# Kernel optimization log

Measured on AMD Instinct MI355X. Metric: run time of the kernel, lower is better.

## Reference

```python
import jax, jax.numpy as jnp
import numpy as np

B, S, D, H = 4, 2048, 1024, 16
DK = D // H

def setup_inputs() -> dict:
    key = jax.random.key(0)
    ks = jax.random.split(key, 8)
    Q = jax.random.normal(ks[0], (B, S, D), dtype=jnp.float32)
    K = jax.random.normal(ks[1], (B, S, D), dtype=jnp.float32)
    V = jax.random.normal(ks[2], (B, S, D), dtype=jnp.float32)
    # causal mask: 0 means masked (as in masked_fill(mask == 0, -inf))
    mask = jnp.broadcast_to(jnp.tril(jnp.ones((S, S), dtype=jnp.int32))[None, None], (B, 1, S, S))
    scale = 1.0 / np.sqrt(D)
    W_Q = jax.random.normal(ks[3], (D, D), dtype=jnp.float32) * scale
    W_K = jax.random.normal(ks[4], (D, D), dtype=jnp.float32) * scale
    W_V = jax.random.normal(ks[5], (D, D), dtype=jnp.float32) * scale
    W_O = jax.random.normal(ks[6], (D, D), dtype=jnp.float32) * scale
    return {"Q": Q, "K": K, "V": V, "mask": mask,
            "W_Q": W_Q, "W_K": W_K, "W_V": W_V, "W_O": W_O}

def _split_heads(x):
    # [B, S, D] -> [B, H, S, DK]
    b, s, _ = x.shape
    return x.reshape(b, s, H, DK).transpose(0, 2, 1, 3)

def reference(Q, K, V, mask, W_Q, W_K, W_V, W_O):
    # nn.Linear(d,d,bias=False): y = x @ W.T ; here W_* stored as [D, D]
    q = _split_heads(Q @ W_Q.T)
    k = _split_heads(K @ W_K.T)
    v = _split_heads(V @ W_V.T)
    scores = jnp.einsum('bhqd,bhkd->bhqk', q, k) / jnp.sqrt(jnp.float32(DK))
    scores = jnp.where(mask == 0, -jnp.inf, scores)
    weights = jax.nn.softmax(scores, axis=-1)
    weights = jnp.nan_to_num(weights, nan=0.0)  # fully-masked rows -> 0
    # dropout is identity at eval / p=0
    attn = jnp.einsum('bhqk,bhkd->bhqd', weights, v)
    attn = attn.transpose(0, 2, 1, 3).reshape(Q.shape[0], Q.shape[1], D)
    return attn @ W_O.T
```

## Files before the change

kernel.cpp:

```cpp
#include <hip/hip_runtime.h>
#include <stdint.h>

#define B_  4
#define S_  2048
#define D_  1024
#define H_  16
#define DK_ 64

typedef __attribute__((ext_vector_type(8)))  short   short8;
typedef __attribute__((ext_vector_type(8)))  unsigned short ushort8;
typedef __attribute__((ext_vector_type(4)))  float   f32x4;
typedef __attribute__((ext_vector_type(16))) float   f32x16;

#define GPTR(p) ((const __attribute__((address_space(1))) void*)(p))
#define SPTR(p) ((__attribute__((address_space(3))) void*)(p))

__device__ inline unsigned short f2bf(float f) {
  uint32_t u = __float_as_uint(f);
  uint32_t r = (u + 0x7fffu + ((u >> 16) & 1u)) >> 16;
  return (unsigned short)r;
}
__device__ inline float bf2f(unsigned short h) {
  return __uint_as_float(((uint32_t)h) << 16);
}
__device__ inline uint32_t pkbf(float a, float b) {
  uint32_t r;
  asm("v_cvt_pk_bf16_f32 %0, %1, %2" : "=v"(r) : "v"(a), "v"(b));
  return r;
}
__device__ inline short8 mk8(uint32_t a, uint32_t b, uint32_t c, uint32_t d) {
  union { uint32_t u[4]; short8 s; } x;
  x.u[0] = a; x.u[1] = b; x.u[2] = c; x.u[3] = d;
  return x.s;
}

__global__ __launch_bounds__(256) void conv_one(const float* __restrict__ src,
                                                unsigned short* __restrict__ dst,
                                                size_t n) {
  size_t i = ((size_t)blockIdx.x * blockDim.x + threadIdx.x) * 4;
  if (i < n) {
    float4 v = *reinterpret_cast<const float4*>(src + i);
    ushort4 o;
    o.x = f2bf(v.x); o.y = f2bf(v.y); o.z = f2bf(v.z); o.w = f2bf(v.w);
    *reinterpret_cast<ushort4*>(dst + i) = o;
  }
}

__global__ __launch_bounds__(256) void conv_x3(const float* __restrict__ q,
                                               const float* __restrict__ k,
                                               const float* __restrict__ v,
                                               unsigned short* __restrict__ dst) {
  const size_t NX = (size_t)B_ * S_ * D_;
  const float* src = (blockIdx.z == 0) ? q : (blockIdx.z == 1) ? k : v;
  unsigned short* d = dst + (size_t)blockIdx.z * NX;
  size_t i = ((size_t)blockIdx.x * blockDim.x + threadIdx.x) * 4;
  float4 vv = *reinterpret_cast<const float4*>(src + i);
  ushort4 o;
  o.x = f2bf(vv.x); o.y = f2bf(vv.y); o.z = f2bf(vv.z); o.w = f2bf(vv.w);
  *reinterpret_cast<ushort4*>(d + i) = o;
}

__global__ __launch_bounds__(256) void conv_w4(const float* __restrict__ w0,
                                               const float* __restrict__ w1,
                                               const float* __restrict__ w2,
                                               const float* __restrict__ w3,
                                               unsigned short* __restrict__ dst) {
  const size_t NW = (size_t)D_ * D_;
  const float* src = (blockIdx.z == 0) ? w0 : (blockIdx.z == 1) ? w1
                   : (blockIdx.z == 2) ? w2 : w3;
  unsigned short* d = dst + (size_t)blockIdx.z * NW;
  size_t i = ((size_t)blockIdx.x * blockDim.x + threadIdx.x) * 4;
  if (i < NW) {
    float4 v = *reinterpret_cast<const float4*>(src + i);
    ushort4 o;
    o.x = f2bf(v.x); o.y = f2bf(v.y); o.z = f2bf(v.z); o.w = f2bf(v.w);
    *reinterpret_cast<ushort4*>(d + i) = o;
  }
}

#define BM 128
#define BN 128
#define BK 32

__global__ __launch_bounds__(256) void gemm_qkv(const unsigned short* __restrict__ X0,
                                                const unsigned short* __restrict__ X1,
                                                const unsigned short* __restrict__ X2,
                                                const unsigned short* __restrict__ W,
                                                unsigned short* __restrict__ P,
                                                int zbase) {
  const size_t NW = (size_t)D_ * D_;
  const size_t NX = (size_t)B_ * S_ * D_;
  const int z = zbase + blockIdx.z;

  const unsigned short* A;
  const unsigned short* Bm;
  unsigned short* C;
  int N, m0, n0;
  if (z == 2) {
    A = W + 2 * NW; Bm = X2; C = P + 2 * NX;
    N = B_ * S_;
    m0 = (blockIdx.x & 7) * BM;
    n0 = (blockIdx.x >> 3) * BN;
  } else {
    A = z ? X1 : X0; Bm = W + (size_t)z * NW; C = P + (size_t)z * NX;
    N = D_;
    m0 = (blockIdx.x >> 3) * BM;
    n0 = (blockIdx.x & 7) * BN;
  }
  const int K = D_;

  __shared__ unsigned short sA[BM * BK];
  __shared__ unsigned short sB[BN * BK];

  const int tid  = threadIdx.x;
  const int lane = tid & 63;
  const int wid  = tid >> 6;
  const int wr   = wid >> 1, wc = wid & 1;
  const int g = lane >> 4, c = lane & 15;

  f32x4 acc[4][4];
#pragma unroll
  for (int m = 0; m < 4; ++m)
#pragma unroll
    for (int n = 0; n < 4; ++n) acc[m][n] = (f32x4){0.f, 0.f, 0.f, 0.f};

  const int nkt = K / BK;
  for (int kt = 0; kt < nkt; ++kt) {
    const int k0 = kt * BK;
#pragma unroll
    for (int i = 0; i < 2; ++i) {
      const int ob  = i * 4096 + wid * 1024 + lane * 16;
      const int row = ob >> 6;
      const int cb  = ob & 63;
      const unsigned short* ga = A  + (size_t)(m0 + row) * K + k0 + (cb >> 1);
      const unsigned short* gb = Bm + (size_t)(n0 + row) * K + k0 + (cb >> 1);
      __builtin_amdgcn_global_load_lds(GPTR(ga), SPTR(&sA[(i * 4096 + wid * 1024) >> 1]), 16, 0, 0);
      __builtin_amdgcn_global_load_lds(GPTR(gb), SPTR(&sB[(i * 4096 + wid * 1024) >> 1]), 16, 0, 0);
    }
    __syncthreads();

    short8 af[4], bf[4];
#pragma unroll
    for (int m = 0; m < 4; ++m)
      af[m] = *reinterpret_cast<const short8*>(&sA[(wr * 64 + m * 16 + c) * BK + 8 * g]);
#pragma unroll
    for (int n = 0; n < 4; ++n)
      bf[n] = *reinterpret_cast<const short8*>(&sB[(wc * 64 + n * 16 + c) * BK + 8 * g]);
#pragma unroll
    for (int m = 0; m < 4; ++m)
#pragma unroll
      for (int n = 0; n < 4; ++n)
        acc[m][n] = __builtin_amdgcn_mfma_f32_16x16x32_bf16(af[m], bf[n], acc[m][n], 0, 0, 0);
    __syncthreads();
  }

#pragma unroll
  for (int m = 0; m < 4; ++m)
#pragma unroll
    for (int n = 0; n < 4; ++n)
#pragma unroll
      for (int r = 0; r < 4; ++r) {
        const int row = m0 + wr * 64 + m * 16 + 4 * g + r;
        const int col = n0 + wc * 64 + n * 16 + c;
        C[(size_t)row * N + col] = f2bf(acc[m][n][r]);
      }
}

__global__ __launch_bounds__(256) void gemm_out(const unsigned short* __restrict__ A,
                                                const unsigned short* __restrict__ Bm,
                                                float* __restrict__ C,
                                                int M, int N, int K) {
  __shared__ unsigned short sA[BM * BK];
  __shared__ unsigned short sB[BN * BK];

  const int tid  = threadIdx.x;
  const int lane = tid & 63;
  const int wid  = tid >> 6;
  const int wr   = wid >> 1, wc = wid & 1;
  const int g = lane >> 4, c = lane & 15;

  const int m0 = blockIdx.y * BM;
  const int n0 = blockIdx.x * BN;

  f32x4 acc[4][4];
#pragma unroll
  for (int m = 0; m < 4; ++m)
#pragma unroll
    for (int n = 0; n < 4; ++n) acc[m][n] = (f32x4){0.f, 0.f, 0.f, 0.f};

  const int nkt = K / BK;
  for (int kt = 0; kt < nkt; ++kt) {
    const int k0 = kt * BK;
#pragma unroll
    for (int i = 0; i < 2; ++i) {
      const int ob  = i * 4096 + wid * 1024 + lane * 16;
      const int row = ob >> 6;
      const int cb  = ob & 63;
      const unsigned short* ga = A  + (size_t)(m0 + row) * K + k0 + (cb >> 1);
      const unsigned short* gb = Bm + (size_t)(n0 + row) * K + k0 + (cb >> 1);
      __builtin_amdgcn_global_load_lds(GPTR(ga), SPTR(&sA[(i * 4096 + wid * 1024) >> 1]), 16, 0, 0);
      __builtin_amdgcn_global_load_lds(GPTR(gb), SPTR(&sB[(i * 4096 + wid * 1024) >> 1]), 16, 0, 0);
    }
    __syncthreads();

    short8 af[4], bf[4];
#pragma unroll
    for (int m = 0; m < 4; ++m)
      af[m] = *reinterpret_cast<const short8*>(&sA[(wr * 64 + m * 16 + c) * BK + 8 * g]);
#pragma unroll
    for (int n = 0; n < 4; ++n)
      bf[n] = *reinterpret_cast<const short8*>(&sB[(wc * 64 + n * 16 + c) * BK + 8 * g]);
#pragma unroll
    for (int m = 0; m < 4; ++m)
#pragma unroll
      for (int n = 0; n < 4; ++n)
        acc[m][n] = __builtin_amdgcn_mfma_f32_16x16x32_bf16(af[m], bf[n], acc[m][n], 0, 0, 0);
    __syncthreads();
  }

#pragma unroll
  for (int m = 0; m < 4; ++m)
#pragma unroll
    for (int n = 0; n < 4; ++n)
#pragma unroll
      for (int r = 0; r < 4; ++r) {
        const int row = m0 + wr * 64 + m * 16 + 4 * g + r;
        const int col = n0 + wc * 64 + n * 16 + c;
        C[(size_t)row * N + col] = acc[m][n][r];
      }
}

__global__ __launch_bounds__(256, 4) void attn_fwd(const unsigned short* __restrict__ qp,
                                                   const unsigned short* __restrict__ kp,
                                                   const unsigned short* __restrict__ vtp,
                                                   unsigned short* __restrict__ attn) {
  const int bx = blockIdx.x;
  const int bh = blockIdx.y;
  const int b = bh >> 4, h = bh & 15;

  __shared__ unsigned short smem[4 * 64 * 64];

  const int tid  = threadIdx.x;
  const int lane = tid & 63;
  const int wid  = tid >> 6;
  const int hi   = lane >> 5;
  const int lo5  = lane & 31;

  const size_t headoff  = (size_t)b * S_ * D_ + (size_t)h * DK_;
  const size_t vheadoff = (size_t)(h * DK_) * (size_t)(B_ * S_) + (size_t)b * S_;

  const int xk = (lo5 & 7) << 4;

  auto stage = [&](int kt_, int bs) {
#pragma unroll
    for (int i = 0; i < 2; ++i) {
      const int base_ob = i * 4096 + wid * 1024;
      const int ob  = base_ob + lane * 16;
      const int row = ob >> 7;
      const int scb = (ob & 127) ^ ((row & 7) << 4);
      const unsigned short* gk = &kp[headoff + (size_t)(kt_ * 64 + row) * D_ + (scb >> 1)];
      const unsigned short* gv = &vtp[vheadoff + (size_t)row * (B_ * S_) + kt_ * 64 + (scb >> 1)];
      __builtin_amdgcn_global_load_lds(GPTR(gk), SPTR(&smem[bs * 4096 + (base_ob >> 1)]), 16, 0, 0);
      __builtin_amdgcn_global_load_lds(GPTR(gv), SPTR(&smem[8192 + bs * 4096 + (base_ob >> 1)]), 16, 0, 0);
    }
  };

#pragma unroll 1
  for (int pass = 0; pass < 2; ++pass) {
    const int qtile = pass ? bx : (15 - bx);
    const int qw = qtile * 128 + wid * 32;
    const int qg = qw + lo5;

    __syncthreads();

    short8 aq[4];
#pragma unroll
    for (int t = 0; t < 4; ++t) {
      ushort8 raw = *reinterpret_cast<const ushort8*>(
          &qp[headoff + (size_t)qg * D_ + t * 16 + hi * 8]);
      short8 sv;
#pragma unroll
      for (int j = 0; j < 8; ++j) sv[j] = (short)f2bf(bf2f(raw[j]) * 0.125f);
      aq[t] = sv;
    }

    float mrun = -3.0e38f, lrun = 0.f;
    f32x16 oa0, oa1;
#pragma unroll
    for (int r = 0; r < 16; ++r) { oa0[r] = 0.f; oa1[r] = 0.f; }

    const int nkv = 2 * (qtile + 1);
    stage(0, 0);

    for (int kt = 0; kt < nkv; ++kt) {
      const int cur = kt & 1;
      if (kt < nkv - 1) {
        stage(kt + 1, cur ^ 1);
        asm volatile("s_waitcnt vmcnt(4)" ::: "memory");
      } else {
        asm volatile("s_waitcnt vmcnt(0)" ::: "memory");
      }
      __builtin_amdgcn_sched_barrier(0);
      __builtin_amdgcn_s_barrier();
      __builtin_amdgcn_sched_barrier(0);

      const int kv0 = kt * 64;
      if (kv0 <= qw + 31) {
        const unsigned short* Kb = &smem[cur * 4096];
        const unsigned short* Vb = &smem[8192 + cur * 4096];

        f32x16 st0, st1;
#pragma unroll
        for (int r = 0; r < 16; ++r) { st0[r] = 0.f; st1[r] = 0.f; }
        __builtin_amdgcn_s_setprio(1);
#pragma unroll
        for (int t = 0; t < 4; ++t) {
          const int off = ((32 * t + 16 * hi) ^ xk) >> 1;
          short8 k0 = *reinterpret_cast<const short8*>(&Kb[lo5 * 64 + off]);
          short8 k1 = *reinterpret_cast<const short8*>(&Kb[(32 + lo5) * 64 + off]);
          st0 = __builtin_amdgcn_mfma_f32_32x32x16_bf16(k0, aq[t], st0, 0, 0, 0);
          st1 = __builtin_amdgcn_mfma_f32_32x32x16_bf16(k1, aq[t], st1, 0, 0, 0);
        }
        __builtin_amdgcn_s_setprio(0);

        if (kv0 + 63 > qw) {
#pragma unroll
          for (int r = 0; r < 16; ++r) {
            const int kvl = kv0 + (r & 3) + 8 * (r >> 2) + 4 * hi;
            if (kvl > qg)      st0[r] = -3.0e38f;
            if (kvl + 32 > qg) st1[r] = -3.0e38f;
          }
        }

        float tm = fmaxf(st0[0], st1[0]);
#pragma unroll
        for (int r = 1; r < 16; ++r) tm = fmaxf(tm, fmaxf(st0[r], st1[r]));
        tm = fmaxf(tm, __shfl_xor(tm, 32));
        const float newm = fmaxf(mrun, tm);
        const float alpha = __expf(mrun - newm);
        mrun = newm;

        float ls = 0.f;
#pragma unroll
        for (int r = 0; r < 16; ++r) { st0[r] = __expf(st0[r] - newm); ls += st0[r]; }
        uint32_t w0a = pkbf(st0[0],  st0[1]),  w0b = pkbf(st0[2],  st0[3]);
        uint32_t w1a = pkbf(st0[4],  st0[5]),  w1b = pkbf(st0[6],  st0[7]);
        uint32_t w2a = pkbf(st0[8],  st0[9]),  w2b = pkbf(st0[10], st0[11]);
        uint32_t w3a = pkbf(st0[12], st0[13]), w3b = pkbf(st0[14], st0[15]);
        uint32_t s0a = (uint32_t)__shfl_xor((int)w0a, 32), s0b = (uint32_t)__shfl_xor((int)w0b, 32);
        uint32_t s1a = (uint32_t)__shfl_xor((int)w1a, 32), s1b = (uint32_t)__shfl_xor((int)w1b, 32);
        uint32_t s2a = (uint32_t)__shfl_xor((int)w2a, 32), s2b = (uint32_t)__shfl_xor((int)w2b, 32);
        uint32_t s3a = (uint32_t)__shfl_xor((int)w3a, 32), s3b = (uint32_t)__shfl_xor((int)w3b, 32);
        short8 pf0 = hi ? mk8(s1a, s1b, w1a, w1b) : mk8(w0a, w0b, s0a, s0b);
        short8 pf1 = hi ? mk8(s3a, s3b, w3a, w3b) : mk8(w2a, w2b, s2a, s2b);

#pragma unroll
        for (int r = 0; r < 16; ++r) { st1[r] = __expf(st1[r] - newm); ls += st1[r]; }
        uint32_t x0a = pkbf(st1[0],  st1[1]),  x0b = pkbf(st1[2],  st1[3]);
        uint32_t x1a = pkbf(st1[4],  st1[5]),  x1b = pkbf(st1[6],  st1[7]);
        uint32_t x2a = pkbf(st1[8],  st1[9]),  x2b = pkbf(st1[10], st1[11]);
        uint32_t x3a = pkbf(st1[12], st1[13]), x3b = pkbf(st1[14], st1[15]);
        uint32_t y0a = (uint32_t)__shfl_xor((int)x0a, 32), y0b = (uint32_t)__shfl_xor((int)x0b, 32);
        uint32_t y1a = (uint32_t)__shfl_xor((int)x1a, 32), y1b = (uint32_t)__shfl_xor((int)x1b, 32);
        uint32_t y2a = (uint32_t)__shfl_xor((int)x2a, 32), y2b = (uint32_t)__shfl_xor((int)x2b, 32);
        uint32_t y3a = (uint32_t)__shfl_xor((int)x3a, 32), y3b = (uint32_t)__shfl_xor((int)x3b, 32);
        short8 pf2 = hi ? mk8(y1a, y1b, x1a, x1b) : mk8(x0a, x0b, y0a, y0b);
        short8 pf3 = hi ? mk8(y3a, y3b, x3a, x3b) : mk8(x2a, x2b, y2a, y2b);

        ls += __shfl_xor(ls, 32);
        lrun = lrun * alpha + ls;

#pragma unroll
        for (int r = 0; r < 16; ++r) { oa0[r] *= alpha; oa1[r] *= alpha; }

        __builtin_amdgcn_s_setprio(1);
#pragma unroll
        for (int c4 = 0; c4 < 4; ++c4) {
          const int off = ((32 * c4 + 16 * hi) ^ xk) >> 1;
          short8 v0 = *reinterpret_cast<const short8*>(&Vb[lo5 * 64 + off]);
          short8 v1 = *reinterpret_cast<const short8*>(&Vb[(32 + lo5) * 64 + off]);
          const short8 pf = (c4 == 0) ? pf0 : (c4 == 1) ? pf1 : (c4 == 2) ? pf2 : pf3;
          oa0 = __builtin_amdgcn_mfma_f32_32x32x16_bf16(v0, pf, oa0, 0, 0, 0);
          oa1 = __builtin_amdgcn_mfma_f32_32x32x16_bf16(v1, pf, oa1, 0, 0, 0);
        }
        __builtin_amdgcn_s_setprio(0);
      }

      asm volatile("s_waitcnt lgkmcnt(0)" ::: "memory");
      __builtin_amdgcn_sched_barrier(0);
      __builtin_amdgcn_s_barrier();
      __builtin_amdgcn_sched_barrier(0);
    }

    {
      unsigned short* sO = &smem[wid * (32 * 72)];
      const float inv = 1.0f / lrun;
#pragma unroll
      for (int r = 0; r < 16; ++r) {
        const int dl = (r & 3) + 8 * (r >> 2) + 4 * hi;
        sO[lo5 * 72 + dl]      = f2bf(oa0[r] * inv);
        sO[lo5 * 72 + 32 + dl] = f2bf(oa1[r] * inv);
      }
      asm volatile("s_waitcnt lgkmcnt(0)" ::: "memory");
      const int row = lane >> 1, h2 = lane & 1;
      const unsigned short* src = &smem[wid * (32 * 72) + row * 72 + h2 * 32];
      unsigned short* dst = &attn[headoff + (size_t)(qtile * 128 + wid * 32 + row) * D_ + h2 * 32];
#pragma unroll
      for (int j = 0; j < 4; ++j)
        *reinterpret_cast<short8*>(dst + 8 * j) = *reinterpret_cast<const short8*>(src + 8 * j);
    }
  }
}

extern "C" void kernel_launch(void* const* d_in, const int* in_sizes, int n_in,
                              void* d_out, int out_size, void* d_ws, size_t ws_size,
                              hipStream_t stream) {
  const float* Q  = (const float*)d_in[0];
  const float* K  = (const float*)d_in[1];
  const float* V  = (const float*)d_in[2];
  const float* Wq = (const float*)d_in[4];
  const float* Wk = (const float*)d_in[5];
  const float* Wv = (const float*)d_in[6];
  const float* Wo = (const float*)d_in[7];
  float* out = (float*)d_out;

  const size_t NX = (size_t)B_ * S_ * D_;
  const size_t NW = (size_t)D_ * D_;

  const bool fused = ws_size >= 2 * (6 * NX + 4 * NW);

  unsigned short* ws = (unsigned short*)d_ws;
  unsigned short* Xq = ws;
  unsigned short* Xk = fused ? Xq + NX : Xq;
  unsigned short* Xv = fused ? Xk + NX : Xq;
  unsigned short* Wb = Xv + NX;
  unsigned short* Pj = Wb + 4 * NW;
  unsigned short* At = Xq;

  const int M = B_ * S_;
  dim3 blk(256);
  dim3 gridConvX((unsigned)(NX / 4 / 256), 1, 3);
  dim3 gridConvW((unsigned)(NW / 4 / 256), 1, 4);
  dim3 gridQKV(512, 1, 3);
  dim3 gridOut(D_ / BN, M / BM);
  dim3 gridAttn(8, B_ * H_);

  conv_w4<<<gridConvW, blk, 0, stream>>>(Wq, Wk, Wv, Wo, Wb);

  if (fused) {
    conv_x3<<<gridConvX, blk, 0, stream>>>(Q, K, V, Xq);
    gemm_qkv<<<gridQKV, blk, 0, stream>>>(Xq, Xk, Xv, Wb, Pj, 0);
  } else {
    dim3 g1((unsigned)(NX / 4 / 256));
    dim3 gz(512, 1, 1);
    conv_one<<<g1, blk, 0, stream>>>(Q, Xq, NX);
    gemm_qkv<<<gz, blk, 0, stream>>>(Xq, Xq, Xq, Wb, Pj, 0);
    conv_one<<<g1, blk, 0, stream>>>(K, Xq, NX);
    gemm_qkv<<<gz, blk, 0, stream>>>(Xq, Xq, Xq, Wb, Pj, 1);
    conv_one<<<g1, blk, 0, stream>>>(V, Xq, NX);
    gemm_qkv<<<gz, blk, 0, stream>>>(Xq, Xq, Xq, Wb, Pj, 2);
  }

  attn_fwd<<<gridAttn, blk, 0, stream>>>(Pj, Pj + NX, Pj + 2 * NX, At);
  gemm_out<<<gridOut, blk, 0, stream>>>(At, Wb + 3 * NW, out, M, D_, D_);
}
```

Measured before the change: 216.9 us.

## Double-buffer GEMM LDS tiles, lazy softmax rescale, permlane swap, reorder attention grid

Both projection GEMMs now use two LDS buffers and prefetch the next K tile while computing the current one, so global loads overlap with MFMA work. In attention, the online-softmax rescale is skipped unless the tile max exceeds the running max by more than a threshold. Cross-half P fragment exchange now uses v_permlane32_swap instead of shuffles. The attention grid is transposed so heads vary fastest. Costs are doubled LDS use in the GEMMs and a wider exponent range in the un-rescaled softmax path.

```diff
diff --git a/kernel.cpp b/kernel.cpp
--- a/kernel.cpp
+++ b/kernel.cpp
@@ -27,6 +27,9 @@
   uint32_t r;
   asm("v_cvt_pk_bf16_f32 %0, %1, %2" : "=v"(r) : "v"(a), "v"(b));
   return r;
+}
+__device__ inline void pl32(uint32_t& a, uint32_t& b) {
+  asm volatile("v_permlane32_swap_b32 %0, %1" : "+v"(a), "+v"(b));
 }
 __device__ inline short8 mk8(uint32_t a, uint32_t b, uint32_t c, uint32_t d) {
   union { uint32_t u[4]; short8 s; } x;
@@ -109,8 +112,8 @@
   }
   const int K = D_;
 
-  __shared__ unsigned short sA[BM * BK];
-  __shared__ unsigned short sB[BN * BK];
+  __shared__ unsigned short sA[2][BM * BK];
+  __shared__ unsigned short sB[2][BN * BK];
 
   const int tid  = threadIdx.x;
   const int lane = tid & 63;
@@ -124,9 +127,8 @@
 #pragma unroll
     for (int n = 0; n < 4; ++n) acc[m][n] = (f32x4){0.f, 0.f, 0.f, 0.f};
 
-  const int nkt = K / BK;
-  for (int kt = 0; kt < nkt; ++kt) {
-    const int k0 = kt * BK;
+  auto stage = [&](int kt_, int bs) {
+    const int k0 = kt_ * BK;
 #pragma unroll
     for (int i = 0; i < 2; ++i) {
       const int ob  = i * 4096 + wid * 1024 + lane * 16;
@@ -134,24 +136,32 @@
       const int cb  = ob & 63;
       const unsigned short* ga = A  + (size_t)(m0 + row) * K + k0 + (cb >> 1);
       const unsigned short* gb = Bm + (size_t)(n0 + row) * K + k0 + (cb >> 1);
-      __builtin_amdgcn_global_load_lds(GPTR(ga), SPTR(&sA[(i * 4096 + wid * 1024) >> 1]), 16, 0, 0);
-      __builtin_amdgcn_global_load_lds(GPTR(gb), SPTR(&sB[(i * 4096 + wid * 1024) >> 1]), 16, 0, 0);
-    }
-    __syncthreads();
+      __builtin_amdgcn_global_load_lds(GPTR(ga), SPTR(&sA[bs][(i * 4096 + wid * 1024) >> 1]), 16, 0, 0);
+      __builtin_amdgcn_global_load_lds(GPTR(gb), SPTR(&sB[bs][(i * 4096 + wid * 1024) >> 1]), 16, 0, 0);
+    }
+  };
+
+  const int nkt = K / BK;
+  stage(0, 0);
+  __syncthreads();
+  int cur = 0;
+  for (int kt = 0; kt < nkt; ++kt) {
+    if (kt + 1 < nkt) stage(kt + 1, cur ^ 1);
 
     short8 af[4], bf[4];
 #pragma unroll
     for (int m = 0; m < 4; ++m)
-      af[m] = *reinterpret_cast<const short8*>(&sA[(wr * 64 + m * 16 + c) * BK + 8 * g]);
+      af[m] = *reinterpret_cast<const short8*>(&sA[cur][(wr * 64 + m * 16 + c) * BK + 8 * g]);
 #pragma unroll
     for (int n = 0; n < 4; ++n)
-      bf[n] = *reinterpret_cast<const short8*>(&sB[(wc * 64 + n * 16 + c) * BK + 8 * g]);
+      bf[n] = *reinterpret_cast<const short8*>(&sB[cur][(wc * 64 + n * 16 + c) * BK + 8 * g]);
 #pragma unroll
     for (int m = 0; m < 4; ++m)
 #pragma unroll
       for (int n = 0; n < 4; ++n)
         acc[m][n] = __builtin_amdgcn_mfma_f32_16x16x32_bf16(af[m], bf[n], acc[m][n], 0, 0, 0);
     __syncthreads();
+    cur ^= 1;
   }
 
 #pragma unroll
@@ -170,8 +180,8 @@
                                                 const unsigned short* __restrict__ Bm,
                                                 float* __restrict__ C,
                                                 int M, int N, int K) {
-  __shared__ unsigned short sA[BM * BK];
-  __shared__ unsigned short sB[BN * BK];
+  __shared__ unsigned short sA[2][BM * BK];
+  __shared__ unsigned short sB[2][BN * BK];
 
   const int tid  = threadIdx.x;
   const int lane = tid & 63;
@@ -188,9 +198,8 @@
 #pragma unroll
     for (int n = 0; n < 4; ++n) acc[m][n] = (f32x4){0.f, 0.f, 0.f, 0.f};
 
-  const int nkt = K / BK;
-  for (int kt = 0; kt < nkt; ++kt) {
-    const int k0 = kt * BK;
+  auto stage = [&](int kt_, int bs) {
+    const int k0 = kt_ * BK;
 #pragma unroll
     for (int i = 0; i < 2; ++i) {
       const int ob  = i * 4096 + wid * 1024 + lane * 16;
@@ -198,24 +207,32 @@
       const int cb  = ob & 63;
       const unsigned short* ga = A  + (size_t)(m0 + row) * K + k0 + (cb >> 1);
       const unsigned short* gb = Bm + (size_t)(n0 + row) * K + k0 + (cb >> 1);
-      __builtin_amdgcn_global_load_lds(GPTR(ga), SPTR(&sA[(i * 4096 + wid * 1024) >> 1]), 16, 0, 0);
-      __builtin_amdgcn_global_load_lds(GPTR(gb), SPTR(&sB[(i * 4096 + wid * 1024) >> 1]), 16, 0, 0);
-    }
-    __syncthreads();
+      __builtin_amdgcn_global_load_lds(GPTR(ga), SPTR(&sA[bs][(i * 4096 + wid * 1024) >> 1]), 16, 0, 0);
+      __builtin_amdgcn_global_load_lds(GPTR(gb), SPTR(&sB[bs][(i * 4096 + wid * 1024) >> 1]), 16, 0, 0);
+    }
+  };
+
+  const int nkt = K / BK;
+  stage(0, 0);
+  __syncthreads();
+  int cur = 0;
+  for (int kt = 0; kt < nkt; ++kt) {
+    if (kt + 1 < nkt) stage(kt + 1, cur ^ 1);
 
     short8 af[4], bf[4];
 #pragma unroll
     for (int m = 0; m < 4; ++m)
-      af[m] = *reinterpret_cast<const short8*>(&sA[(wr * 64 + m * 16 + c) * BK + 8 * g]);
+      af[m] = *reinterpret_cast<const short8*>(&sA[cur][(wr * 64 + m * 16 + c) * BK + 8 * g]);
 #pragma unroll
     for (int n = 0; n < 4; ++n)
-      bf[n] = *reinterpret_cast<const short8*>(&sB[(wc * 64 + n * 16 + c) * BK + 8 * g]);
+      bf[n] = *reinterpret_cast<const short8*>(&sB[cur][(wc * 64 + n * 16 + c) * BK + 8 * g]);
 #pragma unroll
     for (int m = 0; m < 4; ++m)
 #pragma unroll
       for (int n = 0; n < 4; ++n)
         acc[m][n] = __builtin_amdgcn_mfma_f32_16x16x32_bf16(af[m], bf[n], acc[m][n], 0, 0, 0);
     __syncthreads();
+    cur ^= 1;
   }
 
 #pragma unroll
@@ -234,8 +251,8 @@
                                                    const unsigned short* __restrict__ kp,
                                                    const unsigned short* __restrict__ vtp,
                                                    unsigned short* __restrict__ attn) {
-  const int bx = blockIdx.x;
-  const int bh = blockIdx.y;
+  const int bh = blockIdx.x;
+  const int bx = blockIdx.y;
   const int b = bh >> 4, h = bh & 15;
 
   __shared__ unsigned short smem[4 * 64 * 64];
@@ -336,42 +353,45 @@
 #pragma unroll
         for (int r = 1; r < 16; ++r) tm = fmaxf(tm, fmaxf(st0[r], st1[r]));
         tm = fmaxf(tm, __shfl_xor(tm, 32));
-        const float newm = fmaxf(mrun, tm);
-        const float alpha = __expf(mrun - newm);
-        mrun = newm;
+        const bool grow = !__all(tm <= mrun + 8.0f);
+        float alpha = 1.0f;
+        if (grow) {
+          const float newm = fmaxf(mrun, tm);
+          alpha = __expf(mrun - newm);
+          mrun = newm;
+        }
 
         float ls = 0.f;
 #pragma unroll
-        for (int r = 0; r < 16; ++r) { st0[r] = __expf(st0[r] - newm); ls += st0[r]; }
-        uint32_t w0a = pkbf(st0[0],  st0[1]),  w0b = pkbf(st0[2],  st0[3]);
-        uint32_t w1a = pkbf(st0[4],  st0[5]),  w1b = pkbf(st0[6],  st0[7]);
-        uint32_t w2a = pkbf(st0[8],  st0[9]),  w2b = pkbf(st0[10], st0[11]);
-        uint32_t w3a = pkbf(st0[12], st0[13]), w3b = pkbf(st0[14], st0[15]);
-        uint32_t s0a = (uint32_t)__shfl_xor((int)w0a, 32), s0b = (uint32_t)__shfl_xor((int)w0b, 32);
-        uint32_t s1a = (uint32_t)__shfl_xor((int)w1a, 32), s1b = (uint32_t)__shfl_xor((int)w1b, 32);
-        uint32_t s2a = (uint32_t)__shfl_xor((int)w2a, 32), s2b = (uint32_t)__shfl_xor((int)w2b, 32);
-        uint32_t s3a = (uint32_t)__shfl_xor((int)w3a, 32), s3b = (uint32_t)__shfl_xor((int)w3b, 32);
-        short8 pf0 = hi ? mk8(s1a, s1b, w1a, w1b) : mk8(w0a, w0b, s0a, s0b);
-        short8 pf1 = hi ? mk8(s3a, s3b, w3a, w3b) : mk8(w2a, w2b, s2a, s2b);
-
-#pragma unroll
-        for (int r = 0; r < 16; ++r) { st1[r] = __expf(st1[r] - newm); ls += st1[r]; }
-        uint32_t x0a = pkbf(st1[0],  st1[1]),  x0b = pkbf(st1[2],  st1[3]);
-        uint32_t x1a = pkbf(st1[4],  st1[5]),  x1b = pkbf(st1[6],  st1[7]);
-        uint32_t x2a = pkbf(st1[8],  st1[9]),  x2b = pkbf(st1[10], st1[11]);
-        uint32_t x3a = pkbf(st1[12], st1[13]), x3b = pkbf(st1[14], st1[15]);
-        uint32_t y0a = (uint32_t)__shfl_xor((int)x0a, 32), y0b = (uint32_t)__shfl_xor((int)x0b, 32);
-        uint32_t y1a = (uint32_t)__shfl_xor((int)x1a, 32), y1b = (uint32_t)__shfl_xor((int)x1b, 32);
-        uint32_t y2a = (uint32_t)__shfl_xor((int)x2a, 32), y2b = (uint32_t)__shfl_xor((int)x2b, 32);
-        uint32_t y3a = (uint32_t)__shfl_xor((int)x3a, 32), y3b = (uint32_t)__shfl_xor((int)x3b, 32);
-        short8 pf2 = hi ? mk8(y1a, y1b, x1a, x1b) : mk8(x0a, x0b, y0a, y0b);
-        short8 pf3 = hi ? mk8(y3a, y3b, x3a, x3b) : mk8(x2a, x2b, y2a, y2b);
+        for (int r = 0; r < 16; ++r) { st0[r] = __expf(st0[r] - mrun); ls += st0[r]; }
+        uint32_t a0 = pkbf(st0[0],  st0[1]),  a1 = pkbf(st0[2],  st0[3]);
+        uint32_t b0 = pkbf(st0[4],  st0[5]),  b1 = pkbf(st0[6],  st0[7]);
+        uint32_t c0 = pkbf(st0[8],  st0[9]),  c1 = pkbf(st0[10], st0[11]);
+        uint32_t d0 = pkbf(st0[12], st0[13]), d1 = pkbf(st0[14], st0[15]);
+        pl32(a0, b0); pl32(a1, b1);
+        pl32(c0, d0); pl32(c1, d1);
+        short8 pf0 = mk8(a0, a1, b0, b1);
+        short8 pf1 = mk8(c0, c1, d0, d1);
+
+#pragma unroll
+        for (int r = 0; r < 16; ++r) { st1[r] = __expf(st1[r] - mrun); ls += st1[r]; }
+        uint32_t e0 = pkbf(st1[0],  st1[1]),  e1 = pkbf(st1[2],  st1[3]);
+        uint32_t f0 = pkbf(st1[4],  st1[5]),  f1 = pkbf(st1[6],  st1[7]);
+        uint32_t g0 = pkbf(st1[8],  st1[9]),  g1 = pkbf(st1[10], st1[11]);
+        uint32_t h0 = pkbf(st1[12], st1[13]), h1 = pkbf(st1[14], st1[15]);
+        pl32(e0, f0); pl32(e1, f1);
+        pl32(g0, h0); pl32(g1, h1);
+        short8 pf2 = mk8(e0, e1, f0, f1);
+        short8 pf3 = mk8(g0, g1, h0, h1);
 
         ls += __shfl_xor(ls, 32);
-        lrun = lrun * alpha + ls;
-
-#pragma unroll
-        for (int r = 0; r < 16; ++r) { oa0[r] *= alpha; oa1[r] *= alpha; }
+        if (grow) {
+          lrun = lrun * alpha + ls;
+#pragma unroll
+          for (int r = 0; r < 16; ++r) { oa0[r] *= alpha; oa1[r] *= alpha; }
+        } else {
+          lrun += ls;
+        }
 
         __builtin_amdgcn_s_setprio(1);
 #pragma unroll
@@ -443,7 +463,7 @@
   dim3 gridConvW((unsigned)(NW / 4 / 256), 1, 4);
   dim3 gridQKV(512, 1, 3);
   dim3 gridOut(D_ / BN, M / BM);
-  dim3 gridAttn(8, B_ * H_);
+  dim3 gridAttn(B_ * H_, 8);
 
   conv_w4<<<gridConvW, blk, 0, stream>>>(Wq, Wk, Wv, Wo, Wb);
 
```

New measurement: 208.9 us. 1.04x faster.
